# Kernel optimization log

Measured on AMD Instinct MI355X. Metric: run time of the kernel, lower is better.

The kernel has to match this reference:

```python
import jax, jax.numpy as jnp
import numpy as np

N = 16384      # bag size (samples per quantification bag)
DIN = 128      # raw input feature dim
F = 128        # feature_extraction_module.output_size
BINS = 32      # n_bins
H1, H2 = 1024, 512
NC = 10        # n_classes
SIGMA = 100.0  # soft-histogram steepness


def setup_inputs() -> dict:
    key = jax.random.key(0)
    ks = jax.random.split(key, 6)
    w = lambda k, shp: (jax.random.normal(k, shp, jnp.float32) * 0.02)
    return {
        "x": jax.random.normal(ks[0], (N, DIN), jnp.float32),
        "W_feat": w(ks[1], (DIN, F)),
        "b_feat": jnp.zeros((F,), jnp.float32),
        "W1": w(ks[2], (F * BINS, H1)),
        "b1": jnp.zeros((H1,), jnp.float32),
        "W2": w(ks[3], (H1, H2)),
        "b2": jnp.zeros((H2,), jnp.float32),
        "W3": w(ks[4], (H2, NC)),
        "b3": jnp.zeros((NC,), jnp.float32),
    }


def _soft_histogram(s):
    # s: [N, F] values in (0,1). Uniform bins over [0,1].
    delta = 1.0 / BINS
    centers = (jnp.arange(BINS, dtype=s.dtype) + 0.5) * delta  # [BINS]
    d = s[:, :, None] - centers  # [N, F, BINS]  (fusion target)
    soft = jax.nn.sigmoid(SIGMA * (d + 0.5 * delta)) - jax.nn.sigmoid(SIGMA * (d - 0.5 * delta))
    return jnp.mean(soft, axis=0)  # [F, BINS] normalized counts


def reference(x, W_feat, b_feat, W1, b1, W2, b2, W3, b3):
    feats = x @ W_feat + b_feat                 # [N, F] feature extraction
    s = jax.nn.sigmoid(feats)                   # Sigmoid layer -> (0,1)
    hist = _soft_histogram(s).reshape(F * BINS) # differentiable histogram, flattened
    h = jax.nn.leaky_relu(hist @ W1 + b1)       # Linear + LeakyReLU (Dropout p=0 -> identity)
    h = jax.nn.leaky_relu(h @ W2 + b2)
    logits = h @ W3 + b3                        # [NC]
    return jax.nn.softmax(logits, axis=0)       # Softmax(dim=0) over classes
```

## Files before the change

kernel.cpp:

```cpp
#include <hip/hip_runtime.h>
#include <math.h>

#define N_SAMP 16384
#define DIN 128
#define FDIM 128
#define BINS 32
#define NEDGE 33
#define CELLS (FDIM * NEDGE)
#define H1 1024
#define H2 512
#define NC 10

#define K1_BLOCKS 1024
#define K1_ROWS 16
#define K1_THREADS 256
#define XSS 132
#define WTS 136

#define K3_BLOCKS 256
#define EXP_3_125 22.7598950f

typedef __attribute__((ext_vector_type(8))) short bf16x8;
typedef __attribute__((ext_vector_type(4))) float f32x4;

__device__ __forceinline__ float sig_from_t(float t) {
    return __builtin_amdgcn_rcpf(1.f + t);
}
__device__ __forceinline__ float lrelu(float x) { return x > 0.f ? x : 0.01f * x; }
__device__ __forceinline__ unsigned short f2bf(float f) {
    unsigned int u = __float_as_uint(f);
    u += 0x7FFF + ((u >> 16) & 1);
    return (unsigned short)(u >> 16);
}

template <int NE>
__device__ __forceinline__ void sig_chain(float z0neg, float* locE) {
    float tt = __expf(z0neg);
    #pragma unroll
    for (int j = 0; j < NE; ++j) {
        locE[j] += sig_from_t(tt);
        tt *= EXP_3_125;
    }
}

__global__ __launch_bounds__(256) void k0_wfT(
    const float* __restrict__ Wf, unsigned int* __restrict__ wfT_g)
{
    __shared__ unsigned short tile[8 * 128];
    const int b = blockIdx.x;
    const int t = threadIdx.x;
    const int k = t & 127, half = t >> 7;
    #pragma unroll
    for (int j = 0; j < 4; ++j) {
        const int nj = half * 4 + j;
        tile[nj * 128 + k] = f2bf(Wf[k * FDIM + b * 8 + nj]);
    }
    __syncthreads();
    const unsigned int* tl = (const unsigned int*)tile;
    #pragma unroll
    for (int j = 0; j < 2; ++j) {
        const int d = t + 256 * j;
        const int nj = d >> 6, kd = d & 63;
        wfT_g[(size_t)(b * 8 + nj) * 64 + kd] = tl[nj * 64 + kd];
    }
}

__global__ __launch_bounds__(K1_THREADS, 4) void k1_feat_hist(
    const float* __restrict__ x, const unsigned int* __restrict__ wfT_g,
    const float* __restrict__ bfeat, float* __restrict__ E_part)
{
    __shared__ float xs[K1_ROWS * XSS];
    __shared__ unsigned short wfT[FDIM * WTS];
    const int t = threadIdx.x, blk = blockIdx.x;
    const int row0 = blk * K1_ROWS;

    {
        int r = t >> 5, c4 = (t & 31) << 2;
        *(float4*)&xs[r * XSS + c4] = *(const float4*)(x + (size_t)(row0 + r) * DIN + c4);
        const int i1 = t + 256;
        r = i1 >> 5; c4 = (i1 & 31) << 2;
        *(float4*)&xs[r * XSS + c4] = *(const float4*)(x + (size_t)(row0 + r) * DIN + c4);
    }
    {
        unsigned int* wd = (unsigned int*)wfT;
        #pragma unroll
        for (int j = 0; j < 8; ++j) {
            const int p = t + 256 * j;
            const int n = p >> 4, k16 = (p & 15) << 2;
            const uint4 v = *(const uint4*)(wfT_g + (size_t)n * 64 + k16);
            *(uint4*)&wd[n * (WTS / 2) + k16] = v;
        }
    }
    __syncthreads();

    const int w = t >> 6, L = t & 63;
    const int m = L & 15, q = L >> 4;

    bf16x8 afr[4];
    #pragma unroll
    for (int kc = 0; kc < 4; ++kc) {
        const float* ap = &xs[m * XSS + kc * 32 + q * 8];
        const float4 a0 = *(const float4*)ap;
        const float4 a1 = *(const float4*)(ap + 4);
        bf16x8 af;
        af[0] = (short)f2bf(a0.x); af[1] = (short)f2bf(a0.y);
        af[2] = (short)f2bf(a0.z); af[3] = (short)f2bf(a0.w);
        af[4] = (short)f2bf(a1.x); af[5] = (short)f2bf(a1.y);
        af[6] = (short)f2bf(a1.z); af[7] = (short)f2bf(a1.w);
        afr[kc] = af;
    }

    f32x4 acc0 = {0.f, 0.f, 0.f, 0.f}, acc1 = {0.f, 0.f, 0.f, 0.f};
    #pragma unroll
    for (int kc = 0; kc < 4; ++kc) {
        const bf16x8 b0 = *(const bf16x8*)&wfT[(w * 32 + m) * WTS + kc * 32 + q * 8];
        const bf16x8 b1 = *(const bf16x8*)&wfT[(w * 32 + 16 + m) * WTS + kc * 32 + q * 8];
        acc0 = __builtin_amdgcn_mfma_f32_16x16x32_bf16(afr[kc], b0, acc0, 0, 0, 0);
        acc1 = __builtin_amdgcn_mfma_f32_16x16x32_bf16(afr[kc], b1, acc1, 0, 0, 0);
    }

    __syncthreads();

    {
        const int f0 = w * 32 + m;
        const float bias0 = bfeat[f0], bias1 = bfeat[f0 + 16];
        #pragma unroll
        for (int r = 0; r < 4; ++r) {
            const int row = q * 4 + r;
            xs[row * XSS + f0]      = sig_from_t(__expf(-(acc0[r] + bias0)));
            xs[row * XSS + f0 + 16] = sig_from_t(__expf(-(acc1[r] + bias1)));
        }
    }
    __syncthreads();

    const int feat = t & 127;
    const int eg = t >> 7;
    const int estart = eg ? 17 : 0;
    const int ne = eg ? 16 : 17;
    const float c0 = 3.125f * (float)estart;

    float locE[17];
    #pragma unroll
    for (int j = 0; j < 17; ++j) locE[j] = 0.f;

    for (int r = 0; r < K1_ROWS; ++r) {
        const float z100 = 100.f * xs[r * XSS + feat];
        if (eg == 0) sig_chain<17>(c0 - z100, locE);
        else         sig_chain<16>(c0 - z100, locE);
    }

    float* dst = E_part + (size_t)blk * CELLS + feat * NEDGE + estart;
    for (int j = 0; j < ne; ++j) dst[j] = locE[j];
}

__global__ __launch_bounds__(256) void k2_reduce(
    const float* __restrict__ E_part, float* __restrict__ E32)
{
    const int cell = blockIdx.x * 256 + threadIdx.x;
    if (cell >= CELLS) return;
    const int g = blockIdx.y;
    const float* p = E_part + (size_t)g * 32 * CELLS + cell;
    float a0 = 0, a1 = 0, a2 = 0, a3 = 0;
    #pragma unroll
    for (int q = 0; q < 32; q += 4) {
        a0 += p[(size_t)(q + 0) * CELLS];
        a1 += p[(size_t)(q + 1) * CELLS];
        a2 += p[(size_t)(q + 2) * CELLS];
        a3 += p[(size_t)(q + 3) * CELLS];
    }
    E32[g * CELLS + cell] = (a0 + a1) + (a2 + a3);
}

__global__ __launch_bounds__(256) void k3_h1(
    const float* __restrict__ E32, const float* __restrict__ W1,
    float* __restrict__ h1_part)
{
    const int b = blockIdx.x, t = threadIdx.x;
    const int f = b >> 1, bin0 = (b & 1) * 16;
    const int c0 = f * NEDGE + bin0;

    float4 w[16];
    #pragma unroll
    for (int k = 0; k < 16; ++k)
        w[k] = *(const float4*)(W1 + (size_t)(b * 16 + k) * H1 + t * 4);

    __shared__ float hl[17];
    if (t < 17) {
        const float* p = E32 + c0 + t;
        float a0 = 0, a1 = 0, a2 = 0, a3 = 0;
        #pragma unroll
        for (int g = 0; g < 32; g += 4) {
            a0 += p[(size_t)(g + 0) * CELLS];
            a1 += p[(size_t)(g + 1) * CELLS];
            a2 += p[(size_t)(g + 2) * CELLS];
            a3 += p[(size_t)(g + 3) * CELLS];
        }
        hl[t] = (a0 + a1) + (a2 + a3);
    }
    __syncthreads();

    float4 acc = {0, 0, 0, 0};
    #pragma unroll
    for (int k = 0; k < 16; ++k) {
        const float h = (hl[k] - hl[k + 1]) * (1.f / (float)N_SAMP);
        acc.x = fmaf(h, w[k].x, acc.x);
        acc.y = fmaf(h, w[k].y, acc.y);
        acc.z = fmaf(h, w[k].z, acc.z);
        acc.w = fmaf(h, w[k].w, acc.w);
    }
    *(float4*)(h1_part + (size_t)b * H1 + t * 4) = acc;
}

__global__ __launch_bounds__(128) void k5_h2(
    const float* __restrict__ h1_part, const float* __restrict__ b1,
    const float* __restrict__ W2, float* __restrict__ h2_part)
{
    const int b = blockIdx.x, t = threadIdx.x;

    float4 w[8];
    #pragma unroll
    for (int k = 0; k < 8; ++k)
        w[k] = *(const float4*)(W2 + (size_t)(b * 8 + k) * H2 + t * 4);

    __shared__ float hred[8 * 16];
    __shared__ float hv[8];
    const int col = t & 7, q = t >> 3;
    {
        const float* p0 = h1_part + (size_t)(q * 16) * H1 + b * 8 + col;
        float a0 = 0, a1 = 0, a2 = 0, a3 = 0;
        #pragma unroll
        for (int p = 0; p < 16; p += 4) {
            a0 += p0[(size_t)(p + 0) * H1];
            a1 += p0[(size_t)(p + 1) * H1];
            a2 += p0[(size_t)(p + 2) * H1];
            a3 += p0[(size_t)(p + 3) * H1];
        }
        hred[col * 16 + q] = (a0 + a1) + (a2 + a3);
    }
    __syncthreads();
    if (t < 8) {
        float s = 0.f;
        #pragma unroll
        for (int q2 = 0; q2 < 16; ++q2) s += hred[t * 16 + q2];
        hv[t] = lrelu(s + b1[b * 8 + t]);
    }
    __syncthreads();

    float4 acc = {0, 0, 0, 0};
    #pragma unroll
    for (int k = 0; k < 8; ++k) {
        const float h = hv[k];
        acc.x = fmaf(h, w[k].x, acc.x);
        acc.y = fmaf(h, w[k].y, acc.y);
        acc.z = fmaf(h, w[k].z, acc.z);
        acc.w = fmaf(h, w[k].w, acc.w);
    }
    *(float4*)(h2_part + (size_t)b * H2 + t * 4) = acc;
}

__global__ __launch_bounds__(512) void k6_final(
    const float* __restrict__ h2_part, const float* __restrict__ b2,
    const float* __restrict__ W3, const float* __restrict__ b3,
    float* __restrict__ out)
{
    const int t = threadIdx.x;
    float a0 = 0, a1 = 0, a2 = 0, a3 = 0;
    #pragma unroll 8
    for (int p = 0; p < 128; p += 4) {
        a0 += h2_part[(size_t)(p + 0) * H2 + t];
        a1 += h2_part[(size_t)(p + 1) * H2 + t];
        a2 += h2_part[(size_t)(p + 2) * H2 + t];
        a3 += h2_part[(size_t)(p + 3) * H2 + t];
    }
    const float h2v = lrelu(((a0 + a1) + (a2 + a3)) + b2[t]);

    float lc[NC];
    #pragma unroll
    for (int c = 0; c < NC; ++c) lc[c] = h2v * W3[t * NC + c];
    #pragma unroll
    for (int off = 32; off >= 1; off >>= 1) {
        #pragma unroll
        for (int c = 0; c < NC; ++c) lc[c] += __shfl_down(lc[c], off, 64);
    }

    __shared__ float wsum[8][NC];
    if ((t & 63) == 0) {
        #pragma unroll
        for (int c = 0; c < NC; ++c) wsum[t >> 6][c] = lc[c];
    }
    __syncthreads();

    if (t == 0) {
        float logits[NC];
        float m = -1e30f;
        #pragma unroll
        for (int c = 0; c < NC; ++c) {
            float v = b3[c];
            for (int ww = 0; ww < 8; ++ww) v += wsum[ww][c];
            logits[c] = v;
            m = fmaxf(m, v);
        }
        float ssum = 0.f;
        #pragma unroll
        for (int c = 0; c < NC; ++c) { logits[c] = __expf(logits[c] - m); ssum += logits[c]; }
        const float inv = 1.f / ssum;
        #pragma unroll
        for (int c = 0; c < NC; ++c) out[c] = logits[c] * inv;
    }
}

extern "C" void kernel_launch(void* const* d_in, const int* in_sizes, int n_in,
                              void* d_out, int out_size, void* d_ws, size_t ws_size,
                              hipStream_t stream)
{
    const float* x  = (const float*)d_in[0];
    const float* Wf = (const float*)d_in[1];
    const float* bf = (const float*)d_in[2];
    const float* W1 = (const float*)d_in[3];
    const float* b1 = (const float*)d_in[4];
    const float* W2 = (const float*)d_in[5];
    const float* b2 = (const float*)d_in[6];
    const float* W3 = (const float*)d_in[7];
    const float* b3 = (const float*)d_in[8];
    float* out = (float*)d_out;

    float* ws      = (float*)d_ws;
    float* E_part  = ws;
    float* E32     = E_part + (size_t)K1_BLOCKS * CELLS;
    float* h1_part = E32 + (size_t)32 * CELLS;
    float* h2_part = h1_part + (size_t)K3_BLOCKS * H1;
    unsigned int* wfT_g = (unsigned int*)(h2_part + 128 * H2);

    k0_wfT<<<16, 256, 0, stream>>>(Wf, wfT_g);
    k1_feat_hist<<<K1_BLOCKS, K1_THREADS, 0, stream>>>(x, wfT_g, bf, E_part);
    k2_reduce<<<dim3(17, 32), 256, 0, stream>>>(E_part, E32);
    k3_h1<<<K3_BLOCKS, 256, 0, stream>>>(E32, W1, h1_part);
    k5_h2<<<128, 128, 0, stream>>>(h1_part, b1, W2, h2_part);
    k6_final<<<1, 512, 0, stream>>>(h2_part, b2, W3, b3, out);
}
```

Baseline: 132.2 us.

## Double rows per feature-hist block, load W_feat fragments directly to registers, transpose E layout

The feature/histogram kernel now processes 32 rows per block across half as many blocks. It converts x to bf16 once into shared memory and keeps the W_feat MFMA B-fragments in registers loaded straight from global, instead of staging the transposed weights in LDS. The partial-histogram layout becomes edge-major so stores and the downstream reads are coalesced. The reduction, h1 and h2 stages are rebalanced to match (16 partials per group, 64 h2 blocks with 16 rows each). The goal is less redundant weight staging and reduction traffic, at the cost of more registers per thread and lower block count and occupancy in the first kernel.

```diff
diff --git a/kernel.cpp b/kernel.cpp
--- a/kernel.cpp
+++ b/kernel.cpp
@@ -11,11 +11,11 @@
 #define H2 512
 #define NC 10
 
-#define K1_BLOCKS 1024
-#define K1_ROWS 16
+#define K1_BLOCKS 512
+#define K1_ROWS 32
 #define K1_THREADS 256
-#define XSS 132
-#define WTS 136
+#define XBS 136
+#define SSS 132
 
 #define K3_BLOCKS 256
 #define EXP_3_125 22.7598950f
@@ -65,71 +65,64 @@
     }
 }
 
-__global__ __launch_bounds__(K1_THREADS, 4) void k1_feat_hist(
+__global__ __launch_bounds__(K1_THREADS, 3) void k1_feat_hist(
     const float* __restrict__ x, const unsigned int* __restrict__ wfT_g,
     const float* __restrict__ bfeat, float* __restrict__ E_part)
 {
-    __shared__ float xs[K1_ROWS * XSS];
-    __shared__ unsigned short wfT[FDIM * WTS];
+    __shared__ unsigned short xbf[K1_ROWS * XBS];
+    __shared__ float s[K1_ROWS * SSS];
     const int t = threadIdx.x, blk = blockIdx.x;
-    const int row0 = blk * K1_ROWS;
-
-    {
-        int r = t >> 5, c4 = (t & 31) << 2;
-        *(float4*)&xs[r * XSS + c4] = *(const float4*)(x + (size_t)(row0 + r) * DIN + c4);
-        const int i1 = t + 256;
-        r = i1 >> 5; c4 = (i1 & 31) << 2;
-        *(float4*)&xs[r * XSS + c4] = *(const float4*)(x + (size_t)(row0 + r) * DIN + c4);
-    }
-    {
-        unsigned int* wd = (unsigned int*)wfT;
-        #pragma unroll
-        for (int j = 0; j < 8; ++j) {
-            const int p = t + 256 * j;
-            const int n = p >> 4, k16 = (p & 15) << 2;
-            const uint4 v = *(const uint4*)(wfT_g + (size_t)n * 64 + k16);
-            *(uint4*)&wd[n * (WTS / 2) + k16] = v;
-        }
-    }
-    __syncthreads();
-
     const int w = t >> 6, L = t & 63;
     const int m = L & 15, q = L >> 4;
 
-    bf16x8 afr[4];
+    bf16x8 bfrag[2][4];
+    #pragma unroll
+    for (int fh = 0; fh < 2; ++fh) {
+        const int n = w * 32 + fh * 16 + m;
+        #pragma unroll
+        for (int kc = 0; kc < 4; ++kc)
+            bfrag[fh][kc] = *(const bf16x8*)(wfT_g + (size_t)n * 64 + kc * 16 + q * 4);
+    }
+
+    const int row0 = blk * K1_ROWS;
+    #pragma unroll
+    for (int i = 0; i < 4; ++i) {
+        const int idx = t + i * 256;
+        const int r = idx >> 5, c4 = (idx & 31) << 2;
+        const float4 v = *(const float4*)(x + (size_t)(row0 + r) * DIN + c4);
+        unsigned short* p = &xbf[r * XBS + c4];
+        p[0] = f2bf(v.x); p[1] = f2bf(v.y); p[2] = f2bf(v.z); p[3] = f2bf(v.w);
+    }
+    __syncthreads();
+
+    f32x4 acc[2][2];
+    #pragma unroll
+    for (int rt = 0; rt < 2; ++rt)
+        #pragma unroll
+        for (int fh = 0; fh < 2; ++fh)
+            acc[rt][fh] = (f32x4){0.f, 0.f, 0.f, 0.f};
+
     #pragma unroll
     for (int kc = 0; kc < 4; ++kc) {
-        const float* ap = &xs[m * XSS + kc * 32 + q * 8];
-        const float4 a0 = *(const float4*)ap;
-        const float4 a1 = *(const float4*)(ap + 4);
-        bf16x8 af;
-        af[0] = (short)f2bf(a0.x); af[1] = (short)f2bf(a0.y);
-        af[2] = (short)f2bf(a0.z); af[3] = (short)f2bf(a0.w);
-        af[4] = (short)f2bf(a1.x); af[5] = (short)f2bf(a1.y);
-        af[6] = (short)f2bf(a1.z); af[7] = (short)f2bf(a1.w);
-        afr[kc] = af;
-    }
-
-    f32x4 acc0 = {0.f, 0.f, 0.f, 0.f}, acc1 = {0.f, 0.f, 0.f, 0.f};
-    #pragma unroll
-    for (int kc = 0; kc < 4; ++kc) {
-        const bf16x8 b0 = *(const bf16x8*)&wfT[(w * 32 + m) * WTS + kc * 32 + q * 8];
-        const bf16x8 b1 = *(const bf16x8*)&wfT[(w * 32 + 16 + m) * WTS + kc * 32 + q * 8];
-        acc0 = __builtin_amdgcn_mfma_f32_16x16x32_bf16(afr[kc], b0, acc0, 0, 0, 0);
-        acc1 = __builtin_amdgcn_mfma_f32_16x16x32_bf16(afr[kc], b1, acc1, 0, 0, 0);
-    }
-
-    __syncthreads();
+        const bf16x8 a0 = *(const bf16x8*)&xbf[m * XBS + kc * 32 + q * 8];
+        const bf16x8 a1 = *(const bf16x8*)&xbf[(16 + m) * XBS + kc * 32 + q * 8];
+        acc[0][0] = __builtin_amdgcn_mfma_f32_16x16x32_bf16(a0, bfrag[0][kc], acc[0][0], 0, 0, 0);
+        acc[0][1] = __builtin_amdgcn_mfma_f32_16x16x32_bf16(a0, bfrag[1][kc], acc[0][1], 0, 0, 0);
+        acc[1][0] = __builtin_amdgcn_mfma_f32_16x16x32_bf16(a1, bfrag[0][kc], acc[1][0], 0, 0, 0);
+        acc[1][1] = __builtin_amdgcn_mfma_f32_16x16x32_bf16(a1, bfrag[1][kc], acc[1][1], 0, 0, 0);
+    }
 
     {
         const int f0 = w * 32 + m;
-        const float bias0 = bfeat[f0], bias1 = bfeat[f0 + 16];
-        #pragma unroll
-        for (int r = 0; r < 4; ++r) {
-            const int row = q * 4 + r;
-            xs[row * XSS + f0]      = sig_from_t(__expf(-(acc0[r] + bias0)));
-            xs[row * XSS + f0 + 16] = sig_from_t(__expf(-(acc1[r] + bias1)));
-        }
+        const float b0v = bfeat[f0], b1v = bfeat[f0 + 16];
+        #pragma unroll
+        for (int rt = 0; rt < 2; ++rt)
+            #pragma unroll
+            for (int r = 0; r < 4; ++r) {
+                const int row = rt * 16 + q * 4 + r;
+                s[row * SSS + f0]      = sig_from_t(__expf(-(acc[rt][0][r] + b0v)));
+                s[row * SSS + f0 + 16] = sig_from_t(__expf(-(acc[rt][1][r] + b1v)));
+            }
     }
     __syncthreads();
 
@@ -144,13 +137,13 @@
     for (int j = 0; j < 17; ++j) locE[j] = 0.f;
 
     for (int r = 0; r < K1_ROWS; ++r) {
-        const float z100 = 100.f * xs[r * XSS + feat];
-        if (eg == 0) sig_chain<17>(c0 - z100, locE);
-        else         sig_chain<16>(c0 - z100, locE);
-    }
-
-    float* dst = E_part + (size_t)blk * CELLS + feat * NEDGE + estart;
-    for (int j = 0; j < ne; ++j) dst[j] = locE[j];
+        const float z0neg = c0 - 100.f * s[r * SSS + feat];
+        if (eg == 0) sig_chain<17>(z0neg, locE);
+        else         sig_chain<16>(z0neg, locE);
+    }
+
+    float* dst = E_part + (size_t)blk * CELLS + estart * FDIM + feat;
+    for (int j = 0; j < ne; ++j) dst[j * FDIM] = locE[j];
 }
 
 __global__ __launch_bounds__(256) void k2_reduce(
@@ -159,14 +152,14 @@
     const int cell = blockIdx.x * 256 + threadIdx.x;
     if (cell >= CELLS) return;
     const int g = blockIdx.y;
-    const float* p = E_part + (size_t)g * 32 * CELLS + cell;
+    const float* p = E_part + (size_t)g * 16 * CELLS + cell;
     float a0 = 0, a1 = 0, a2 = 0, a3 = 0;
     #pragma unroll
-    for (int q = 0; q < 32; q += 4) {
-        a0 += p[(size_t)(q + 0) * CELLS];
-        a1 += p[(size_t)(q + 1) * CELLS];
-        a2 += p[(size_t)(q + 2) * CELLS];
-        a3 += p[(size_t)(q + 3) * CELLS];
+    for (int qq = 0; qq < 16; qq += 4) {
+        a0 += p[(size_t)(qq + 0) * CELLS];
+        a1 += p[(size_t)(qq + 1) * CELLS];
+        a2 += p[(size_t)(qq + 2) * CELLS];
+        a3 += p[(size_t)(qq + 3) * CELLS];
     }
     E32[g * CELLS + cell] = (a0 + a1) + (a2 + a3);
 }
@@ -177,16 +170,15 @@
 {
     const int b = blockIdx.x, t = threadIdx.x;
     const int f = b >> 1, bin0 = (b & 1) * 16;
-    const int c0 = f * NEDGE + bin0;
-
-    float4 w[16];
+
+    float4 wr[16];
     #pragma unroll
     for (int k = 0; k < 16; ++k)
-        w[k] = *(const float4*)(W1 + (size_t)(b * 16 + k) * H1 + t * 4);
+        wr[k] = *(const float4*)(W1 + (size_t)(b * 16 + k) * H1 + t * 4);
 
     __shared__ float hl[17];
     if (t < 17) {
-        const float* p = E32 + c0 + t;
+        const float* p = E32 + (bin0 + t) * FDIM + f;
         float a0 = 0, a1 = 0, a2 = 0, a3 = 0;
         #pragma unroll
         for (int g = 0; g < 32; g += 4) {
@@ -203,10 +195,10 @@
     #pragma unroll
     for (int k = 0; k < 16; ++k) {
         const float h = (hl[k] - hl[k + 1]) * (1.f / (float)N_SAMP);
-        acc.x = fmaf(h, w[k].x, acc.x);
-        acc.y = fmaf(h, w[k].y, acc.y);
-        acc.z = fmaf(h, w[k].z, acc.z);
-        acc.w = fmaf(h, w[k].w, acc.w);
+        acc.x = fmaf(h, wr[k].x, acc.x);
+        acc.y = fmaf(h, wr[k].y, acc.y);
+        acc.z = fmaf(h, wr[k].z, acc.z);
+        acc.w = fmaf(h, wr[k].w, acc.w);
     }
     *(float4*)(h1_part + (size_t)b * H1 + t * 4) = acc;
 }
@@ -217,43 +209,43 @@
 {
     const int b = blockIdx.x, t = threadIdx.x;
 
-    float4 w[8];
-    #pragma unroll
-    for (int k = 0; k < 8; ++k)
-        w[k] = *(const float4*)(W2 + (size_t)(b * 8 + k) * H2 + t * 4);
-
-    __shared__ float hred[8 * 16];
-    __shared__ float hv[8];
-    const int col = t & 7, q = t >> 3;
+    float4 wr[16];
+    #pragma unroll
+    for (int k = 0; k < 16; ++k)
+        wr[k] = *(const float4*)(W2 + (size_t)(b * 16 + k) * H2 + t * 4);
+
+    __shared__ float hred[16 * 8];
+    __shared__ float hv[16];
+    const int c = t & 15, qg = t >> 4;
     {
-        const float* p0 = h1_part + (size_t)(q * 16) * H1 + b * 8 + col;
+        const float* p0 = h1_part + (size_t)(qg * 32) * H1 + b * 16 + c;
         float a0 = 0, a1 = 0, a2 = 0, a3 = 0;
         #pragma unroll
-        for (int p = 0; p < 16; p += 4) {
+        for (int p = 0; p < 32; p += 4) {
             a0 += p0[(size_t)(p + 0) * H1];
             a1 += p0[(size_t)(p + 1) * H1];
             a2 += p0[(size_t)(p + 2) * H1];
             a3 += p0[(size_t)(p + 3) * H1];
         }
-        hred[col * 16 + q] = (a0 + a1) + (a2 + a3);
-    }
-    __syncthreads();
-    if (t < 8) {
-        float s = 0.f;
-        #pragma unroll
-        for (int q2 = 0; q2 < 16; ++q2) s += hred[t * 16 + q2];
-        hv[t] = lrelu(s + b1[b * 8 + t]);
+        hred[c * 8 + qg] = (a0 + a1) + (a2 + a3);
+    }
+    __syncthreads();
+    if (t < 16) {
+        float sum = 0.f;
+        #pragma unroll
+        for (int g = 0; g < 8; ++g) sum += hred[t * 8 + g];
+        hv[t] = lrelu(sum + b1[b * 16 + t]);
     }
     __syncthreads();
 
     float4 acc = {0, 0, 0, 0};
     #pragma unroll
-    for (int k = 0; k < 8; ++k) {
+    for (int k = 0; k < 16; ++k) {
         const float h = hv[k];
-        acc.x = fmaf(h, w[k].x, acc.x);
-        acc.y = fmaf(h, w[k].y, acc.y);
-        acc.z = fmaf(h, w[k].z, acc.z);
-        acc.w = fmaf(h, w[k].w, acc.w);
+        acc.x = fmaf(h, wr[k].x, acc.x);
+        acc.y = fmaf(h, wr[k].y, acc.y);
+        acc.z = fmaf(h, wr[k].z, acc.z);
+        acc.w = fmaf(h, wr[k].w, acc.w);
     }
     *(float4*)(h2_part + (size_t)b * H2 + t * 4) = acc;
 }
@@ -265,8 +257,8 @@
 {
     const int t = threadIdx.x;
     float a0 = 0, a1 = 0, a2 = 0, a3 = 0;
-    #pragma unroll 8
-    for (int p = 0; p < 128; p += 4) {
+    #pragma unroll
+    for (int p = 0; p < 64; p += 4) {
         a0 += h2_part[(size_t)(p + 0) * H2 + t];
         a1 += h2_part[(size_t)(p + 1) * H2 + t];
         a2 += h2_part[(size_t)(p + 2) * H2 + t];
@@ -292,17 +284,17 @@
 
     if (t == 0) {
         float logits[NC];
-        float m = -1e30f;
+        float mx = -1e30f;
         #pragma unroll
         for (int c = 0; c < NC; ++c) {
             float v = b3[c];
             for (int ww = 0; ww < 8; ++ww) v += wsum[ww][c];
             logits[c] = v;
-            m = fmaxf(m, v);
+            mx = fmaxf(mx, v);
         }
         float ssum = 0.f;
         #pragma unroll
-        for (int c = 0; c < NC; ++c) { logits[c] = __expf(logits[c] - m); ssum += logits[c]; }
+        for (int c = 0; c < NC; ++c) { logits[c] = __expf(logits[c] - mx); ssum += logits[c]; }
         const float inv = 1.f / ssum;
         #pragma unroll
         for (int c = 0; c < NC; ++c) out[c] = logits[c] * inv;
@@ -329,12 +321,12 @@
     float* E32     = E_part + (size_t)K1_BLOCKS * CELLS;
     float* h1_part = E32 + (size_t)32 * CELLS;
     float* h2_part = h1_part + (size_t)K3_BLOCKS * H1;
-    unsigned int* wfT_g = (unsigned int*)(h2_part + 128 * H2);
+    unsigned int* wfT_g = (unsigned int*)(h2_part + 64 * H2);
 
     k0_wfT<<<16, 256, 0, stream>>>(Wf, wfT_g);
     k1_feat_hist<<<K1_BLOCKS, K1_THREADS, 0, stream>>>(x, wfT_g, bf, E_part);
     k2_reduce<<<dim3(17, 32), 256, 0, stream>>>(E_part, E32);
     k3_h1<<<K3_BLOCKS, 256, 0, stream>>>(E32, W1, h1_part);
-    k5_h2<<<128, 128, 0, stream>>>(h1_part, b1, W2, h2_part);
+    k5_h2<<<64, 128, 0, stream>>>(h1_part, b1, W2, h2_part);
     k6_final<<<1, 512, 0, stream>>>(h2_part, b2, W3, b3, out);
 }
```

New measurement: 115.0 us. -13.0%, faster.
